# Performance work log

Measured on AMD Instinct MI355X. Metric: run time of the kernel, lower is better.

The kernel has to match this reference:

```python
import jax, jax.numpy as jnp
import numpy as np

EMBED_DIM = 256
NUM_EMB = 4096
COMMIT = 0.25


def setup_inputs() -> dict:
    key = jax.random.key(0)
    k1, k2 = jax.random.split(key)
    inputs = jax.random.normal(k1, (32, 256, 32, 32), dtype=jnp.float32)
    # torch init is uniform(-3, 3); use same scale
    embeddings = jax.random.uniform(k2, (NUM_EMB, EMBED_DIM), dtype=jnp.float32,
                                    minval=-3.0, maxval=3.0)
    return {"inputs": inputs, "embeddings": embeddings, "is_training": 1}


def reference(inputs, embeddings, is_training):
    # inputs: [N, C, H, W] with C == EMBED_DIM; embeddings: [K, C]
    x = jnp.transpose(inputs, (0, 3, 2, 1))          # [N, W, H, C] (torch transpose(1,3))
    flat = x.reshape(-1, EMBED_DIM)                   # [T, C]
    distances = (jnp.sum(flat * flat, axis=1, keepdims=True)
                 - 2.0 * flat @ embeddings.T
                 + jnp.sum(embeddings * embeddings, axis=1)[None, :])
    idx_flat = jnp.argmax(-distances, axis=1)         # [T]
    encodings = jax.nn.one_hot(idx_flat, NUM_EMB, dtype=jnp.float32)  # [T, K]
    encoding_indices = idx_flat.reshape(x.shape[:-1])  # [N, W, H]
    quantized = embeddings[encoding_indices]            # [N, W, H, C]

    e_latent_loss = jnp.mean((jax.lax.stop_gradient(quantized) - x) ** 2)
    q_latent_loss = jnp.mean((quantized - jax.lax.stop_gradient(x)) ** 2)
    loss = q_latent_loss + COMMIT * e_latent_loss

    quantized_st = x + jax.lax.stop_gradient(quantized - x)

    avg_probs = jnp.mean(encodings, axis=0)             # [K]
    perplexity = jnp.exp(-jnp.sum(avg_probs * jnp.log(avg_probs + 1e-10)))

    quantize_out = jnp.transpose(quantized_st, (0, 3, 2, 1))  # back to [N, C, H, W]
    return quantize_out, loss, perplexity, encodings, encoding_indices, distances
```

## Files before the change

kernel.cpp:

```cpp
#include <hip/hip_runtime.h>
#include <math.h>

constexpr int NB = 32, HH = 32, WW = 32, CD = 256, NK = 4096;
constexpr int T_ = NB * WW * HH;
constexpr long long NQ = (long long)NB * CD * HH * WW;
constexpr long long OFF_LOSS = NQ;
constexpr long long OFF_PERP = NQ + 1;
constexpr long long OFF_ENC  = NQ + 2;
constexpr long long ENC_SZ   = (long long)T_ * NK;
constexpr long long OFF_IDX  = OFF_ENC + ENC_SZ;
constexpr long long OFF_DIST = OFF_IDX + T_;
constexpr long long SCR_FLAT = OFF_ENC + 2;
constexpr long long SCR_PVAL = SCR_FLAT + (long long)T_ * CD;
constexpr long long SCR_PIDX = SCR_PVAL + (long long)T_ * 32;

#define TID ((int)threadIdx.x)

__global__ __launch_bounds__(256) void k_transpose(const float* __restrict__ in,
                                                   float* __restrict__ flat) {
  __shared__ float t[256][33];
  int b = blockIdx.x, n = b >> 5, h = b & 31;
  int w = TID & 31, c8 = TID >> 5;
  const float* src = in + (long long)n * 262144 + h * 32;
#pragma unroll
  for (int p = 0; p < 32; ++p) {
    int c = p * 8 + c8;
    t[c][w] = src[c * 1024 + w];
  }
  __syncthreads();
  float* dst = flat + ((long long)n * 1024 + h) * 256;
#pragma unroll
  for (int w2 = 0; w2 < 32; ++w2) dst[w2 * 8192 + TID] = t[TID][w2];
}

__global__ __launch_bounds__(256) void k_rowsq(const float* __restrict__ src,
                                               float* __restrict__ dst, int nrows) {
  int row = blockIdx.x * 4 + (TID >> 6);
  if (row >= nrows) return;
  int lane = TID & 63;
  float4 v = *(const float4*)(src + (long long)row * 256 + lane * 4);
  float s = v.x * v.x + v.y * v.y + v.z * v.z + v.w * v.w;
#pragma unroll
  for (int o = 32; o; o >>= 1) s += __shfl_down(s, o);
  if (lane == 0) dst[row] = s;
}

__global__ __launch_bounds__(256) void k_gemm(const float* __restrict__ A,
                                              const float* __restrict__ B,
                                              const float* __restrict__ xsq,
                                              const float* __restrict__ esq,
                                              float* __restrict__ dist,
                                              float* __restrict__ pval,
                                              int* __restrict__ pidx) {
  __shared__ float As[16][132];
  __shared__ float Bs[16][132];
  int tid = TID;
  int bm = blockIdx.x >> 5, bn = blockIdx.x & 31;
  int tn = tid & 15, tm = tid >> 4;
  int lr = tid >> 2, lk = tid & 3;
  const float* Ag = A + (long long)bm * 128 * 256 + lr * 256 + lk * 4;
  const float* Bg = B + (long long)bn * 128 * 256 + lr * 256 + lk * 4;

  float acc[2][4][2][4] = {};
  for (int kt = 0; kt < 16; ++kt) {
    float4 a0 = *(const float4*)(Ag + kt * 16);
    float4 a1 = *(const float4*)(Ag + 64 * 256 + kt * 16);
    float4 b0 = *(const float4*)(Bg + kt * 16);
    float4 b1 = *(const float4*)(Bg + 64 * 256 + kt * 16);
    __syncthreads();
    As[lk * 4 + 0][lr] = a0.x; As[lk * 4 + 1][lr] = a0.y;
    As[lk * 4 + 2][lr] = a0.z; As[lk * 4 + 3][lr] = a0.w;
    As[lk * 4 + 0][lr + 64] = a1.x; As[lk * 4 + 1][lr + 64] = a1.y;
    As[lk * 4 + 2][lr + 64] = a1.z; As[lk * 4 + 3][lr + 64] = a1.w;
    Bs[lk * 4 + 0][lr] = b0.x; Bs[lk * 4 + 1][lr] = b0.y;
    Bs[lk * 4 + 2][lr] = b0.z; Bs[lk * 4 + 3][lr] = b0.w;
    Bs[lk * 4 + 0][lr + 64] = b1.x; Bs[lk * 4 + 1][lr + 64] = b1.y;
    Bs[lk * 4 + 2][lr + 64] = b1.z; Bs[lk * 4 + 3][lr + 64] = b1.w;
    __syncthreads();
#pragma unroll
    for (int kk = 0; kk < 16; ++kk) {
      float4 av0 = *(const float4*)&As[kk][tm * 4];
      float4 av1 = *(const float4*)&As[kk][64 + tm * 4];
      float4 bv0 = *(const float4*)&Bs[kk][tn * 4];
      float4 bv1 = *(const float4*)&Bs[kk][64 + tn * 4];
      const float* ap0 = &av0.x; const float* ap1 = &av1.x;
      const float* bp0 = &bv0.x; const float* bp1 = &bv1.x;
#pragma unroll
      for (int i = 0; i < 4; ++i)
#pragma unroll
        for (int j = 0; j < 4; ++j) {
          acc[0][i][0][j] = fmaf(ap0[i], bp0[j], acc[0][i][0][j]);
          acc[0][i][1][j] = fmaf(ap0[i], bp1[j], acc[0][i][1][j]);
          acc[1][i][0][j] = fmaf(ap1[i], bp0[j], acc[1][i][0][j]);
          acc[1][i][1][j] = fmaf(ap1[i], bp1[j], acc[1][i][1][j]);
        }
    }
  }
  float4 es0 = *(const float4*)(esq + bn * 128 + tn * 4);
  float4 es1 = *(const float4*)(esq + bn * 128 + 64 + tn * 4);
  const float* ep0 = &es0.x; const float* ep1 = &es1.x;
#pragma unroll
  for (int hh = 0; hh < 2; ++hh)
#pragma unroll
    for (int i = 0; i < 4; ++i) {
      int row = bm * 128 + hh * 64 + tm * 4 + i;
      float xs = xsq[row];
      float dv[8];
#pragma unroll
      for (int j = 0; j < 4; ++j) {
        dv[j]     = xs - 2.0f * acc[hh][i][0][j] + ep0[j];
        dv[4 + j] = xs - 2.0f * acc[hh][i][1][j] + ep1[j];
      }
      float bv = 3.4e38f; int bc = 0;
#pragma unroll
      for (int g = 0; g < 2; ++g)
#pragma unroll
        for (int j = 0; j < 4; ++j) {
          float v = dv[g * 4 + j];
          int c = g * 64 + tn * 4 + j;
          if (v < bv) { bv = v; bc = c; }
        }
      float* drow = dist + (long long)row * 4096 + bn * 128;
      *(float2*)(drow + tn * 4)          = make_float2(dv[0], dv[1]);
      *(float2*)(drow + tn * 4 + 2)      = make_float2(dv[2], dv[3]);
      *(float2*)(drow + 64 + tn * 4)     = make_float2(dv[4], dv[5]);
      *(float2*)(drow + 64 + tn * 4 + 2) = make_float2(dv[6], dv[7]);
#pragma unroll
      for (int m = 1; m < 16; m <<= 1) {
        float ov = __shfl_xor(bv, m);
        int oc = __shfl_xor(bc, m);
        if (ov < bv || (ov == bv && oc < bc)) { bv = ov; bc = oc; }
      }
      if (tn == 0) {
        pval[(long long)row * 32 + bn] = bv;
        pidx[(long long)row * 32 + bn] = bn * 128 + bc;
      }
    }
}

__global__ __launch_bounds__(256) void k_argmin(const float* __restrict__ pval,
                                                const int* __restrict__ pidx,
                                                int* __restrict__ idxArr,
                                                float* __restrict__ outIdx,
                                                int* __restrict__ hist) {
  int t = blockIdx.x * 256 + TID;
  float bv = 3.4e38f; int bc = 0;
#pragma unroll
  for (int b = 0; b < 32; ++b) {
    float v = pval[(long long)t * 32 + b];
    if (v < bv) { bv = v; bc = pidx[(long long)t * 32 + b]; }
  }
  idxArr[t] = bc;
  outIdx[t] = (float)bc;
  atomicAdd(&hist[bc], 1);
}

__global__ __launch_bounds__(256) void k_scatter(const int* __restrict__ idxArr,
                                                 float* __restrict__ enc) {
  int t = blockIdx.x * 256 + TID;
  enc[(long long)t * 4096 + idxArr[t]] = 1.0f;
}

__global__ __launch_bounds__(256) void k_quant(const float* __restrict__ in,
                                               const float* __restrict__ emb,
                                               const int* __restrict__ idxArr,
                                               float* __restrict__ outQ,
                                               float* __restrict__ lossAcc) {
  __shared__ float q[32][257];
  __shared__ float ls[4];
  int b = blockIdx.x, n = b >> 5, h = b & 31;
  for (int w = 0; w < 32; ++w) {
    int id = idxArr[(n * 32 + w) * 32 + h];
    q[w][TID] = emb[(long long)id * 256 + TID];
  }
  __syncthreads();
  float sum = 0.f;
  int w = TID & 31, c8 = TID >> 5;
  const float* xin = in + (long long)n * 262144 + h * 32;
  float* xout = outQ + (long long)n * 262144 + h * 32;
#pragma unroll
  for (int p = 0; p < 32; ++p) {
    int c = p * 8 + c8;
    float qa = q[w][c];
    float xv = xin[c * 1024 + w];
    float d = qa - xv;
    sum += d * d;
    xout[c * 1024 + w] = qa;
  }
#pragma unroll
  for (int o = 32; o; o >>= 1) sum += __shfl_down(sum, o);
  if ((TID & 63) == 0) ls[TID >> 6] = sum;
  __syncthreads();
  if (TID == 0) atomicAdd(lossAcc, ls[0] + ls[1] + ls[2] + ls[3]);
}

__global__ __launch_bounds__(256) void k_final(const int* __restrict__ hist,
                                               const float* __restrict__ lossAcc,
                                               float* __restrict__ outLoss,
                                               float* __restrict__ outPerp) {
  __shared__ float ls[4];
  float s = 0.f;
  for (int k = TID; k < 4096; k += 256) {
    float p = (float)hist[k] * (1.0f / 32768.0f);
    s += p * logf(p + 1e-10f);
  }
#pragma unroll
  for (int o = 32; o; o >>= 1) s += __shfl_down(s, o);
  if ((TID & 63) == 0) ls[TID >> 6] = s;
  __syncthreads();
  if (TID == 0) {
    *outLoss = lossAcc[0] * (1.25f / 8388608.0f);
    *outPerp = expf(-(ls[0] + ls[1] + ls[2] + ls[3]));
  }
}

extern "C" void kernel_launch(void* const* d_in, const int* in_sizes, int n_in,
                              void* d_out, int out_size, void* d_ws, size_t ws_size,
                              hipStream_t stream) {
  const float* inputs = (const float*)d_in[0];
  const float* emb = (const float*)d_in[1];
  float* out = (float*)d_out;
  float* ws = (float*)d_ws;

  float* lossAcc = ws;
  int* hist = (int*)(ws + 64);
  float* xsq = ws + 8192;
  float* esq = ws + 40960;
  int* idxArr = (int*)(ws + 45056);

  float* flat = out + SCR_FLAT;
  float* pval = out + SCR_PVAL;
  int* pidx = (int*)(out + SCR_PIDX);
  float* dist = out + OFF_DIST;
  float* enc = out + OFF_ENC;

  hipMemsetAsync(d_ws, 0, 8192 * 4, stream);
  k_transpose<<<1024, 256, 0, stream>>>(inputs, flat);
  k_rowsq<<<8192, 256, 0, stream>>>(flat, xsq, 32768);
  k_rowsq<<<1024, 256, 0, stream>>>(emb, esq, 4096);
  k_gemm<<<8192, 256, 0, stream>>>(flat, emb, xsq, esq, dist, pval, pidx);
  k_argmin<<<128, 256, 0, stream>>>(pval, pidx, idxArr, out + OFF_IDX, hist);
  hipMemsetAsync(enc, 0, (size_t)ENC_SZ * 4, stream);
  k_scatter<<<128, 256, 0, stream>>>(idxArr, enc);
  k_quant<<<1024, 256, 0, stream>>>(inputs, emb, idxArr, out, lossAcc);
  k_final<<<1, 256, 0, stream>>>(hist, lossAcc, out + OFF_LOSS, out + OFF_PERP);
}
```

Measured before the change: 1.881 ms.

## Prefetch GEMM tiles, transpose partial-argmin layout, fuse one-hot zeroing and scatter

The distance GEMM now prefetches the next K-slice from global memory into registers while computing the current one, keeps accumulators in named float4 registers, and stores distances as float4 with a two-blocks-per-CU launch bound. Partial argmin results are stored column-major so the reduction kernel reads them coalesced. The separate memset and scatter for the 512 MB one-hot matrix are replaced by one kernel that writes zeros and the single one together. Together these aim to hide global load latency, cut uncoalesced traffic, and avoid a second pass over the encodings buffer, at the cost of extra register pressure in the GEMM.

```diff
diff --git a/kernel.cpp b/kernel.cpp
--- a/kernel.cpp
+++ b/kernel.cpp
@@ -45,15 +45,53 @@
   if (lane == 0) dst[row] = s;
 }
 
-__global__ __launch_bounds__(256) void k_gemm(const float* __restrict__ A,
-                                              const float* __restrict__ B,
-                                              const float* __restrict__ xsq,
-                                              const float* __restrict__ esq,
-                                              float* __restrict__ dist,
-                                              float* __restrict__ pval,
-                                              int* __restrict__ pidx) {
-  __shared__ float As[16][132];
-  __shared__ float Bs[16][132];
+#define MK(ci0, ci1, aa)                                          \
+  ci0.x = fmaf(aa, B0.x, ci0.x); ci0.y = fmaf(aa, B0.y, ci0.y);   \
+  ci0.z = fmaf(aa, B0.z, ci0.z); ci0.w = fmaf(aa, B0.w, ci0.w);   \
+  ci1.x = fmaf(aa, B1.x, ci1.x); ci1.y = fmaf(aa, B1.y, ci1.y);   \
+  ci1.z = fmaf(aa, B1.z, ci1.z); ci1.w = fmaf(aa, B1.w, ci1.w);
+
+#define EPI(hh_, ii_, C0, C1) {                                                 \
+  int row = bm * 128 + (hh_) * 64 + tm * 4 + (ii_);                             \
+  float xs = xsq[row];                                                          \
+  float4 dv0, dv1;                                                              \
+  dv0.x = xs - 2.0f * C0.x + ep0.x; dv0.y = xs - 2.0f * C0.y + ep0.y;           \
+  dv0.z = xs - 2.0f * C0.z + ep0.z; dv0.w = xs - 2.0f * C0.w + ep0.w;           \
+  dv1.x = xs - 2.0f * C1.x + ep1.x; dv1.y = xs - 2.0f * C1.y + ep1.y;           \
+  dv1.z = xs - 2.0f * C1.z + ep1.z; dv1.w = xs - 2.0f * C1.w + ep1.w;           \
+  float bv = dv0.x; int bc = tn * 4;                                            \
+  if (dv0.y < bv) { bv = dv0.y; bc = tn * 4 + 1; }                              \
+  if (dv0.z < bv) { bv = dv0.z; bc = tn * 4 + 2; }                              \
+  if (dv0.w < bv) { bv = dv0.w; bc = tn * 4 + 3; }                              \
+  if (dv1.x < bv) { bv = dv1.x; bc = 64 + tn * 4; }                             \
+  if (dv1.y < bv) { bv = dv1.y; bc = 64 + tn * 4 + 1; }                         \
+  if (dv1.z < bv) { bv = dv1.z; bc = 64 + tn * 4 + 2; }                         \
+  if (dv1.w < bv) { bv = dv1.w; bc = 64 + tn * 4 + 3; }                         \
+  float* drow = dist + (long long)row * 4096 + bn * 128;                        \
+  *(float4*)(drow + tn * 4) = dv0;                                              \
+  *(float4*)(drow + 64 + tn * 4) = dv1;                                         \
+  _Pragma("unroll")                                                             \
+  for (int m_ = 1; m_ < 16; m_ <<= 1) {                                         \
+    float ov = __shfl_xor(bv, m_); int oc = __shfl_xor(bc, m_);                 \
+    if (ov < bv || (ov == bv && oc < bc)) { bv = ov; bc = oc; }                 \
+  }                                                                             \
+  if (tn == 0) {                                                                \
+    pval[(long long)bn * 32768 + row] = bv;                                     \
+    pidx[(long long)bn * 32768 + row] = bn * 128 + bc;                          \
+  }                                                                             \
+}
+
+__global__ __launch_bounds__(256, 2) void k_gemm(const float* __restrict__ A,
+                                                 const float* __restrict__ B,
+                                                 const float* __restrict__ xsq,
+                                                 const float* __restrict__ esq,
+                                                 float* __restrict__ dist,
+                                                 float* __restrict__ pval,
+                                                 int* __restrict__ pidx) {
+  __shared__ float4 As4[16][33];
+  __shared__ float4 Bs4[16][33];
+  float* As_s = (float*)As4;
+  float* Bs_s = (float*)Bs4;
   int tid = TID;
   int bm = blockIdx.x >> 5, bn = blockIdx.x & 31;
   int tn = tid & 15, tm = tid >> 4;
@@ -61,81 +99,55 @@
   const float* Ag = A + (long long)bm * 128 * 256 + lr * 256 + lk * 4;
   const float* Bg = B + (long long)bn * 128 * 256 + lr * 256 + lk * 4;
 
-  float acc[2][4][2][4] = {};
+  float4 c000 = {0,0,0,0}, c001 = {0,0,0,0}, c010 = {0,0,0,0}, c011 = {0,0,0,0};
+  float4 c020 = {0,0,0,0}, c021 = {0,0,0,0}, c030 = {0,0,0,0}, c031 = {0,0,0,0};
+  float4 c100 = {0,0,0,0}, c101 = {0,0,0,0}, c110 = {0,0,0,0}, c111 = {0,0,0,0};
+  float4 c120 = {0,0,0,0}, c121 = {0,0,0,0}, c130 = {0,0,0,0}, c131 = {0,0,0,0};
+
+  float4 pa0 = *(const float4*)(Ag);
+  float4 pa1 = *(const float4*)(Ag + 64 * 256);
+  float4 pb0 = *(const float4*)(Bg);
+  float4 pb1 = *(const float4*)(Bg + 64 * 256);
+
   for (int kt = 0; kt < 16; ++kt) {
-    float4 a0 = *(const float4*)(Ag + kt * 16);
-    float4 a1 = *(const float4*)(Ag + 64 * 256 + kt * 16);
-    float4 b0 = *(const float4*)(Bg + kt * 16);
-    float4 b1 = *(const float4*)(Bg + 64 * 256 + kt * 16);
     __syncthreads();
-    As[lk * 4 + 0][lr] = a0.x; As[lk * 4 + 1][lr] = a0.y;
-    As[lk * 4 + 2][lr] = a0.z; As[lk * 4 + 3][lr] = a0.w;
-    As[lk * 4 + 0][lr + 64] = a1.x; As[lk * 4 + 1][lr + 64] = a1.y;
-    As[lk * 4 + 2][lr + 64] = a1.z; As[lk * 4 + 3][lr + 64] = a1.w;
-    Bs[lk * 4 + 0][lr] = b0.x; Bs[lk * 4 + 1][lr] = b0.y;
-    Bs[lk * 4 + 2][lr] = b0.z; Bs[lk * 4 + 3][lr] = b0.w;
-    Bs[lk * 4 + 0][lr + 64] = b1.x; Bs[lk * 4 + 1][lr + 64] = b1.y;
-    Bs[lk * 4 + 2][lr + 64] = b1.z; Bs[lk * 4 + 3][lr + 64] = b1.w;
+    As_s[(lk * 4 + 0) * 132 + lr] = pa0.x; As_s[(lk * 4 + 1) * 132 + lr] = pa0.y;
+    As_s[(lk * 4 + 2) * 132 + lr] = pa0.z; As_s[(lk * 4 + 3) * 132 + lr] = pa0.w;
+    As_s[(lk * 4 + 0) * 132 + 64 + lr] = pa1.x; As_s[(lk * 4 + 1) * 132 + 64 + lr] = pa1.y;
+    As_s[(lk * 4 + 2) * 132 + 64 + lr] = pa1.z; As_s[(lk * 4 + 3) * 132 + 64 + lr] = pa1.w;
+    Bs_s[(lk * 4 + 0) * 132 + lr] = pb0.x; Bs_s[(lk * 4 + 1) * 132 + lr] = pb0.y;
+    Bs_s[(lk * 4 + 2) * 132 + lr] = pb0.z; Bs_s[(lk * 4 + 3) * 132 + lr] = pb0.w;
+    Bs_s[(lk * 4 + 0) * 132 + 64 + lr] = pb1.x; Bs_s[(lk * 4 + 1) * 132 + 64 + lr] = pb1.y;
+    Bs_s[(lk * 4 + 2) * 132 + 64 + lr] = pb1.z; Bs_s[(lk * 4 + 3) * 132 + 64 + lr] = pb1.w;
     __syncthreads();
+    float4 na0 = pa0, na1 = pa1, nb0 = pb0, nb1 = pb1;
+    if (kt < 15) {
+      const float* Ap = Ag + (kt + 1) * 16;
+      const float* Bp = Bg + (kt + 1) * 16;
+      na0 = *(const float4*)(Ap);
+      na1 = *(const float4*)(Ap + 64 * 256);
+      nb0 = *(const float4*)(Bp);
+      nb1 = *(const float4*)(Bp + 64 * 256);
+    }
 #pragma unroll
     for (int kk = 0; kk < 16; ++kk) {
-      float4 av0 = *(const float4*)&As[kk][tm * 4];
-      float4 av1 = *(const float4*)&As[kk][64 + tm * 4];
-      float4 bv0 = *(const float4*)&Bs[kk][tn * 4];
-      float4 bv1 = *(const float4*)&Bs[kk][64 + tn * 4];
-      const float* ap0 = &av0.x; const float* ap1 = &av1.x;
-      const float* bp0 = &bv0.x; const float* bp1 = &bv1.x;
-#pragma unroll
-      for (int i = 0; i < 4; ++i)
-#pragma unroll
-        for (int j = 0; j < 4; ++j) {
-          acc[0][i][0][j] = fmaf(ap0[i], bp0[j], acc[0][i][0][j]);
-          acc[0][i][1][j] = fmaf(ap0[i], bp1[j], acc[0][i][1][j]);
-          acc[1][i][0][j] = fmaf(ap1[i], bp0[j], acc[1][i][0][j]);
-          acc[1][i][1][j] = fmaf(ap1[i], bp1[j], acc[1][i][1][j]);
-        }
+      float4 A0 = As4[kk][tm];
+      float4 A1 = As4[kk][16 + tm];
+      float4 B0 = Bs4[kk][tn];
+      float4 B1 = Bs4[kk][16 + tn];
+      MK(c000, c001, A0.x) MK(c010, c011, A0.y)
+      MK(c020, c021, A0.z) MK(c030, c031, A0.w)
+      MK(c100, c101, A1.x) MK(c110, c111, A1.y)
+      MK(c120, c121, A1.z) MK(c130, c131, A1.w)
     }
-  }
-  float4 es0 = *(const float4*)(esq + bn * 128 + tn * 4);
-  float4 es1 = *(const float4*)(esq + bn * 128 + 64 + tn * 4);
-  const float* ep0 = &es0.x; const float* ep1 = &es1.x;
-#pragma unroll
-  for (int hh = 0; hh < 2; ++hh)
-#pragma unroll
-    for (int i = 0; i < 4; ++i) {
-      int row = bm * 128 + hh * 64 + tm * 4 + i;
-      float xs = xsq[row];
-      float dv[8];
-#pragma unroll
-      for (int j = 0; j < 4; ++j) {
-        dv[j]     = xs - 2.0f * acc[hh][i][0][j] + ep0[j];
-        dv[4 + j] = xs - 2.0f * acc[hh][i][1][j] + ep1[j];
-      }
-      float bv = 3.4e38f; int bc = 0;
-#pragma unroll
-      for (int g = 0; g < 2; ++g)
-#pragma unroll
-        for (int j = 0; j < 4; ++j) {
-          float v = dv[g * 4 + j];
-          int c = g * 64 + tn * 4 + j;
-          if (v < bv) { bv = v; bc = c; }
-        }
-      float* drow = dist + (long long)row * 4096 + bn * 128;
-      *(float2*)(drow + tn * 4)          = make_float2(dv[0], dv[1]);
-      *(float2*)(drow + tn * 4 + 2)      = make_float2(dv[2], dv[3]);
-      *(float2*)(drow + 64 + tn * 4)     = make_float2(dv[4], dv[5]);
-      *(float2*)(drow + 64 + tn * 4 + 2) = make_float2(dv[6], dv[7]);
-#pragma unroll
-      for (int m = 1; m < 16; m <<= 1) {
-        float ov = __shfl_xor(bv, m);
-        int oc = __shfl_xor(bc, m);
-        if (ov < bv || (ov == bv && oc < bc)) { bv = ov; bc = oc; }
-      }
-      if (tn == 0) {
-        pval[(long long)row * 32 + bn] = bv;
-        pidx[(long long)row * 32 + bn] = bn * 128 + bc;
-      }
-    }
+    pa0 = na0; pa1 = na1; pb0 = nb0; pb1 = nb1;
+  }
+  float4 ep0 = *(const float4*)(esq + bn * 128 + tn * 4);
+  float4 ep1 = *(const float4*)(esq + bn * 128 + 64 + tn * 4);
+  EPI(0, 0, c000, c001) EPI(0, 1, c010, c011)
+  EPI(0, 2, c020, c021) EPI(0, 3, c030, c031)
+  EPI(1, 0, c100, c101) EPI(1, 1, c110, c111)
+  EPI(1, 2, c120, c121) EPI(1, 3, c130, c131)
 }
 
 __global__ __launch_bounds__(256) void k_argmin(const float* __restrict__ pval,
@@ -147,18 +159,27 @@
   float bv = 3.4e38f; int bc = 0;
 #pragma unroll
   for (int b = 0; b < 32; ++b) {
-    float v = pval[(long long)t * 32 + b];
-    if (v < bv) { bv = v; bc = pidx[(long long)t * 32 + b]; }
+    float v = pval[(long long)b * 32768 + t];
+    if (v < bv) { bv = v; bc = pidx[(long long)b * 32768 + t]; }
   }
   idxArr[t] = bc;
   outIdx[t] = (float)bc;
   atomicAdd(&hist[bc], 1);
 }
 
-__global__ __launch_bounds__(256) void k_scatter(const int* __restrict__ idxArr,
-                                                 float* __restrict__ enc) {
-  int t = blockIdx.x * 256 + TID;
-  enc[(long long)t * 4096 + idxArr[t]] = 1.0f;
+__global__ __launch_bounds__(256) void k_onehot(const int* __restrict__ idxArr,
+                                                float* __restrict__ enc) {
+  int t0 = blockIdx.x * 8;
+  float4 z = make_float4(0.f, 0.f, 0.f, 0.f);
+#pragma unroll
+  for (int r = 0; r < 8; ++r) {
+    int t = t0 + r;
+    int id = idxArr[t];
+    float* p = enc + (long long)t * 4096 + TID * 16;
+    *(float4*)(p + 0) = z; *(float4*)(p + 4) = z;
+    *(float4*)(p + 8) = z; *(float4*)(p + 12) = z;
+    if ((id >> 4) == TID) p[id & 15] = 1.0f;
+  }
 }
 
 __global__ __launch_bounds__(256) void k_quant(const float* __restrict__ in,
@@ -240,8 +261,7 @@
   k_rowsq<<<1024, 256, 0, stream>>>(emb, esq, 4096);
   k_gemm<<<8192, 256, 0, stream>>>(flat, emb, xsq, esq, dist, pval, pidx);
   k_argmin<<<128, 256, 0, stream>>>(pval, pidx, idxArr, out + OFF_IDX, hist);
-  hipMemsetAsync(enc, 0, (size_t)ENC_SZ * 4, stream);
-  k_scatter<<<128, 256, 0, stream>>>(idxArr, enc);
+  k_onehot<<<4096, 256, 0, stream>>>(idxArr, enc);
   k_quant<<<1024, 256, 0, stream>>>(inputs, emb, idxArr, out, lossAcc);
   k_final<<<1, 256, 0, stream>>>(hist, lossAcc, out + OFF_LOSS, out + OFF_PERP);
 }
```

Measured after the change: 2.001 ms. 1.06x slower.
